# Kernel tuning notes

Measured on AMD Instinct MI355X. Metric: run time of the kernel, lower is better.

## Reference

```python
import jax, jax.numpy as jnp
import numpy as np

NUM_HEADS = 16
HEAD_SIZE = 64
ROPE_THETA = 10000.0


def _rope_tables(T, dim):
    # freqs_cis equivalent: cos/sin tables of shape [T, dim//2]
    inv_freq = 1.0 / (ROPE_THETA ** (jnp.arange(0, dim, 2, dtype=jnp.float32) / dim))
    angle = jnp.arange(T, dtype=jnp.float32)[:, None] * inv_freq[None, :]  # [T, dim/2]
    return jnp.cos(angle), jnp.sin(angle)


def _apply_rope(x, cos, sin):
    # x: [B, H, T, D]; interleaved pairs rotated by angle (complex multiply)
    x2 = x.reshape(*x.shape[:-1], -1, 2)  # [B,H,T,D/2,2]
    x0, x1 = x2[..., 0], x2[..., 1]
    c = cos[None, None, :, :]
    s = sin[None, None, :, :]
    r0 = x0 * c - x1 * s
    r1 = x0 * s + x1 * c
    return jnp.stack([r0, r1], axis=-1).reshape(x.shape)


def setup_inputs() -> dict:
    key = jax.random.key(0)
    ks = jax.random.split(key, 6)
    B, T, C = 4, 2048, 1024
    scale = 1.0 / np.sqrt(C)
    return {
        "x": jax.random.normal(ks[0], (B, T, C), dtype=jnp.float32),
        "Wq": jax.random.normal(ks[1], (C, C), dtype=jnp.float32) * scale,
        "Wk": jax.random.normal(ks[2], (C, C), dtype=jnp.float32) * scale,
        "Wv": jax.random.normal(ks[3], (C, C), dtype=jnp.float32) * scale,
        "Wo": jax.random.normal(ks[4], (C, C), dtype=jnp.float32) * scale,
        "bo": jax.random.normal(ks[5], (C,), dtype=jnp.float32) * 0.01,
    }


def reference(x, Wq, Wk, Wv, Wo, bo):
    B, T, C = x.shape
    H, D = NUM_HEADS, HEAD_SIZE
    # QKV projections (bias-free), split heads -> [B, H, T, D]
    q = (x @ Wq).reshape(B, T, H, D).transpose(0, 2, 1, 3)
    k = (x @ Wk).reshape(B, T, H, D).transpose(0, 2, 1, 3)
    v = (x @ Wv).reshape(B, T, H, D).transpose(0, 2, 1, 3)
    cos, sin = _rope_tables(T, D)
    q = _apply_rope(q, cos, sin)
    k = _apply_rope(k, cos, sin)
    # causal attention with manual stable softmax
    scores = jnp.einsum("bhqd,bhkd->bhqk", q, k) * (D ** -0.5)
    causal = jnp.tril(jnp.ones((T, T), dtype=bool))
    scores = jnp.where(causal[None, None], scores, -jnp.inf)
    probs = jax.nn.softmax(scores, axis=-1)
    out = jnp.einsum("bhqk,bhkd->bhqd", probs, v)  # [B,H,T,D]
    out = out.transpose(0, 2, 1, 3).reshape(B, T, C)
    return out @ Wo + bo
```

## Files before the change

kernel.cpp:

```cpp
#include <hip/hip_runtime.h>
#include <math.h>

#define HH 16
#define DD 64
#define TT 2048
#define BB 4
#define CC 1024
#define MM (BB*TT)

typedef __attribute__((ext_vector_type(8))) short short8;
typedef __attribute__((ext_vector_type(4))) float f32x4;
typedef __attribute__((ext_vector_type(8))) unsigned short bfu8;
typedef __attribute__((ext_vector_type(4))) unsigned short bfu4;

__device__ __forceinline__ unsigned short f2bf(float f) {
    unsigned int u = __builtin_bit_cast(unsigned int, f);
    unsigned int r = (u + 0x7fffu + ((u >> 16) & 1u)) >> 16;
    return (unsigned short)r;
}
__device__ __forceinline__ float bf2f(unsigned short s) {
    unsigned int u = ((unsigned int)s) << 16;
    return __builtin_bit_cast(float, u);
}

__global__ __launch_bounds__(256) void convert_x(
    const float* __restrict__ x, unsigned short* __restrict__ xb)
{
    const size_t i = (size_t)blockIdx.x * 256 + threadIdx.x;
    const float4 a = ((const float4*)x)[i * 2];
    const float4 b = ((const float4*)x)[i * 2 + 1];
    bfu8 o;
    o[0] = f2bf(a.x); o[1] = f2bf(a.y); o[2] = f2bf(a.z); o[3] = f2bf(a.w);
    o[4] = f2bf(b.x); o[5] = f2bf(b.y); o[6] = f2bf(b.z); o[7] = f2bf(b.w);
    *(bfu8*)(xb + i * 8) = o;
}

__global__ __launch_bounds__(256) void transpose_w(
    const float* __restrict__ Wq, const float* __restrict__ Wk,
    const float* __restrict__ Wv, const float* __restrict__ Wo,
    unsigned short* __restrict__ Wt)
{
    __shared__ float st[64][65];
    const int z = blockIdx.z;
    const float* W = (z == 0) ? Wq : (z == 1) ? Wk : (z == 2) ? Wv : Wo;
    unsigned short* out = Wt + (size_t)z * CC * CC;
    const int rb = blockIdx.y * 64, cb = blockIdx.x * 64;
    const int t = threadIdx.x;
    const int tr = t >> 4, tc4 = (t & 15) * 4;
    #pragma unroll
    for (int i = 0; i < 4; ++i) {
        const int r = i * 16 + tr;
        const float4 v = *(const float4*)&W[(size_t)(rb + r) * CC + cb + tc4];
        st[r][tc4 + 0] = v.x; st[r][tc4 + 1] = v.y;
        st[r][tc4 + 2] = v.z; st[r][tc4 + 3] = v.w;
    }
    __syncthreads();
    #pragma unroll
    for (int i = 0; i < 4; ++i) {
        const int c = i * 16 + tr;
        bfu4 o;
        o[0] = f2bf(st[tc4 + 0][c]); o[1] = f2bf(st[tc4 + 1][c]);
        o[2] = f2bf(st[tc4 + 2][c]); o[3] = f2bf(st[tc4 + 3][c]);
        *(bfu4*)&out[(size_t)(cb + c) * CC + rb + tc4] = o;
    }
}

__global__ __launch_bounds__(256) void rope_tables(float2* __restrict__ tab)
{
    const int i = blockIdx.x * 256 + threadIdx.x;
    const int t = i >> 5, p = i & 31;
    const float inv_freq = expf(-(float)(2 * p) * (9.210340371976184f / 64.0f));
    const float ang = (float)t * inv_freq;
    float s, c;
    sincosf(ang, &s, &c);
    tab[i] = make_float2(c, s);
}

__global__ __launch_bounds__(256) void transpose_v(
    const unsigned short* __restrict__ v, unsigned short* __restrict__ vt)
{
    const int bh = blockIdx.y;
    const int t  = blockIdx.x * 256 + threadIdx.x;
    const unsigned short* src = v + ((size_t)bh * TT + t) * DD;
    #pragma unroll
    for (int d0 = 0; d0 < 64; d0 += 8) {
        const bfu8 x = *(const bfu8*)(src + d0);
        #pragma unroll
        for (int j = 0; j < 8; ++j)
            vt[((size_t)bh * DD + d0 + j) * TT + t] = x[j];
    }
}

template<int MODE>
__global__ __launch_bounds__(256) void gemm_mfma(
    const unsigned short* __restrict__ A,
    const unsigned short* __restrict__ Wt,
    const float* __restrict__ bias,
    const float2* __restrict__ tab,
    void* __restrict__ outv)
{
    __shared__ short lds[128 * 32 * 2];
    short* As = lds;
    short* Bs = lds + 128 * 32;

    const int tid  = threadIdx.x;
    const int lane = tid & 63;
    const int w    = tid >> 6;
    const int wr   = w >> 1, wc = w & 1;
    const int mb   = blockIdx.y * 128, nb = blockIdx.x * 128;
    const int z    = (MODE == 1) ? blockIdx.z : 0;
    const unsigned short* Bmat = Wt + (size_t)z * CC * CC;

    f32x4 acc[4][4] = {};

    for (int k0 = 0; k0 < CC; k0 += 32) {
        __syncthreads();
        #pragma unroll
        for (int t2 = 0; t2 < 2; ++t2) {
            const int ci  = w * 128 + t2 * 64 + lane;
            const int row = ci >> 2, kc = ci & 3;
            const unsigned short* ga = A    + (size_t)(mb + row) * CC + k0 + kc * 8;
            const unsigned short* gb = Bmat + (size_t)(nb + row) * CC + k0 + kc * 8;
            __builtin_amdgcn_global_load_lds(
                (const __attribute__((address_space(1))) unsigned int*)ga,
                (__attribute__((address_space(3))) unsigned int*)(As + (w * 2 + t2) * 512),
                16, 0, 0);
            __builtin_amdgcn_global_load_lds(
                (const __attribute__((address_space(1))) unsigned int*)gb,
                (__attribute__((address_space(3))) unsigned int*)(Bs + (w * 2 + t2) * 512),
                16, 0, 0);
        }
        __syncthreads();

        short8 a[4], b[4];
        #pragma unroll
        for (int i = 0; i < 4; ++i) {
            const int ro = (wr * 64 + i * 16 + (lane & 15)) * 32 + (lane >> 4) * 8;
            a[i] = *(const short8*)&As[ro];
            const int co = (wc * 64 + i * 16 + (lane & 15)) * 32 + (lane >> 4) * 8;
            b[i] = *(const short8*)&Bs[co];
        }
        #pragma unroll
        for (int i = 0; i < 4; ++i)
            #pragma unroll
            for (int j = 0; j < 4; ++j)
                acc[i][j] = __builtin_amdgcn_mfma_f32_16x16x32_bf16(
                    a[i], b[j], acc[i][j], 0, 0, 0);
    }

    if (MODE == 0) {
        float* out = (float*)outv;
        #pragma unroll
        for (int i = 0; i < 4; ++i) {
            const int m0 = mb + wr * 64 + i * 16 + (lane >> 4) * 4;
            #pragma unroll
            for (int j = 0; j < 4; ++j) {
                const int n = nb + wc * 64 + j * 16 + (lane & 15);
                const float bv = bias[n];
                #pragma unroll
                for (int r = 0; r < 4; ++r)
                    out[(size_t)(m0 + r) * CC + n] = acc[i][j][r] + bv;
            }
        }
    } else {
        unsigned short* dst = (unsigned short*)outv + (size_t)z * MM * CC;
        const bool do_rope = (z < 2);
        #pragma unroll
        for (int i = 0; i < 4; ++i) {
            const int m0 = mb + wr * 64 + i * 16 + (lane >> 4) * 4;
            #pragma unroll
            for (int j = 0; j < 4; ++j) {
                const int n = nb + wc * 64 + j * 16 + (lane & 15);
                const int h = n >> 6, d = n & 63;
                #pragma unroll
                for (int r = 0; r < 4; ++r) {
                    const int m  = m0 + r;
                    const int b_ = m >> 11, t = m & (TT - 1);
                    const float val     = acc[i][j][r];
                    const float partner = __shfl_xor(val, 1);
                    float r0, r1;
                    if (do_rope) {
                        const float2 cs = tab[t * 32 + (d >> 1)];
                        r0 = val * cs.x - partner * cs.y;
                        r1 = val * cs.y + partner * cs.x;
                    } else {
                        r0 = val; r1 = partner;
                    }
                    if ((lane & 1) == 0) {
                        const unsigned int pk =
                            (unsigned int)f2bf(r0) | ((unsigned int)f2bf(r1) << 16);
                        *(unsigned int*)&dst[(((size_t)(b_ * HH + h) * TT + t) * DD) + (d & ~1)] = pk;
                    }
                }
            }
        }
    }
}

__global__ __launch_bounds__(256) void attn_mfma(
    const unsigned short* __restrict__ qg, const unsigned short* __restrict__ kg,
    const unsigned short* __restrict__ vtg, unsigned short* __restrict__ att)
{
    __shared__ short Ks[2][64 * 64];
    __shared__ short Vs[2][64 * 64];
    __shared__ short Ps[4][16 * 64];

    const int tid  = threadIdx.x;
    const int lane = tid & 63;
    const int w    = tid >> 6;
    const int l15  = lane & 15, l4 = lane >> 4;
    const int qt   = 31 - blockIdx.x;
    const int bh   = blockIdx.y;
    const int qb   = qt * 64;
    const int b_   = bh >> 4, h = bh & 15;

    const unsigned short* qrow = qg + ((size_t)bh * TT + qb + w * 16 + l15) * DD;
    const short8 qf0 = *(const short8*)(qrow + l4 * 8);
    const short8 qf1 = *(const short8*)(qrow + 32 + l4 * 8);

    f32x4 acc_o[4] = {};
    float m_run[4] = {-1e30f, -1e30f, -1e30f, -1e30f};
    float l_run[4] = {};

    const int srow = tid >> 2;
    const int sc0  = (tid & 3) * 16;
    const int bo0  = (srow * 128 + sc0 * 2)       ^ ((srow & 7) << 4);
    const int bo1  = (srow * 128 + (sc0 + 8) * 2) ^ ((srow & 7) << 4);
    const unsigned short* kst = kg  + ((size_t)bh * TT + srow) * DD + sc0;
    const unsigned short* vst = vtg + ((size_t)bh * DD + srow) * TT + sc0;

    const int ntile = qt + 1;

    {
        const short8 k0 = *(const short8*)(kst);
        const short8 k1 = *(const short8*)(kst + 8);
        const short8 v0 = *(const short8*)(vst);
        const short8 v1 = *(const short8*)(vst + 8);
        *(short8*)((char*)&Ks[0][0] + bo0) = k0;
        *(short8*)((char*)&Ks[0][0] + bo1) = k1;
        *(short8*)((char*)&Vs[0][0] + bo0) = v0;
        *(short8*)((char*)&Vs[0][0] + bo1) = v1;
    }
    __syncthreads();

    for (int kt = 0; kt < ntile; ++kt) {
        const int kb  = kt * 64;
        const int cur = kt & 1;
        const short* Kc = &Ks[cur][0];
        const short* Vc = &Vs[cur][0];

        short8 nk0, nk1, nv0, nv1;
        const bool has_next = (kt + 1 < ntile);
        if (has_next) {
            const size_t ko = (size_t)(kb + 64) * DD;
            nk0 = *(const short8*)(kst + ko);
            nk1 = *(const short8*)(kst + ko + 8);
            nv0 = *(const short8*)(vst + kb + 64);
            nv1 = *(const short8*)(vst + kb + 64 + 8);
        }

        f32x4 s4[4];
        __builtin_amdgcn_s_setprio(1);
        #pragma unroll
        for (int kj = 0; kj < 4; ++kj) {
            const int key = kj * 16 + l15;
            const short8 kf0 = *(const short8*)((char*)Kc + ((key * 128 +      l4 * 16) ^ ((key & 7) << 4)));
            const short8 kf1 = *(const short8*)((char*)Kc + ((key * 128 + 64 + l4 * 16) ^ ((key & 7) << 4)));
            f32x4 zz = {};
            zz = __builtin_amdgcn_mfma_f32_16x16x32_bf16(qf0, kf0, zz, 0, 0, 0);
            zz = __builtin_amdgcn_mfma_f32_16x16x32_bf16(qf1, kf1, zz, 0, 0, 0);
            s4[kj] = zz;
        }
        __builtin_amdgcn_s_setprio(0);

        float p[4][4];
        float tmax[4] = {-1e30f, -1e30f, -1e30f, -1e30f};
        const bool diag = (kt == ntile - 1);
        #pragma unroll
        for (int kj = 0; kj < 4; ++kj)
            #pragma unroll
            for (int r = 0; r < 4; ++r) {
                float s = s4[kj][r] * 0.125f;
                if (diag) {
                    const int key_g = kb + kj * 16 + l15;
                    const int q_g   = qb + w * 16 + l4 * 4 + r;
                    if (key_g > q_g) s = -1e30f;
                }
                p[kj][r] = s;
                tmax[r] = fmaxf(tmax[r], s);
            }
        #pragma unroll
        for (int mk = 1; mk < 16; mk <<= 1)
            #pragma unroll
            for (int r = 0; r < 4; ++r)
                tmax[r] = fmaxf(tmax[r], __shfl_xor(tmax[r], mk));

        #pragma unroll
        for (int r = 0; r < 4; ++r) {
            const float mn   = fmaxf(m_run[r], tmax[r]);
            const float corr = __expf(m_run[r] - mn);
            m_run[r] = mn;
            l_run[r] *= corr;
            #pragma unroll
            for (int dj = 0; dj < 4; ++dj) acc_o[dj][r] *= corr;
            float ls = 0.f;
            #pragma unroll
            for (int kj = 0; kj < 4; ++kj) {
                const float e = __expf(p[kj][r] - mn);
                p[kj][r] = e;
                ls += e;
            }
            l_run[r] += ls;
        }

        #pragma unroll
        for (int kj = 0; kj < 4; ++kj)
            #pragma unroll
            for (int r = 0; r < 4; ++r) {
                const int qr  = l4 * 4 + r;
                const int key = kj * 16 + l15;
                const int bo  = (qr * 128 + key * 2) ^ ((qr & 7) << 4);
                *(short*)((char*)&Ps[w][0] + bo) = (short)f2bf(p[kj][r]);
            }

        const short8 pa0 = *(const short8*)((char*)&Ps[w][0] + ((l15 * 128 +      l4 * 16) ^ ((l15 & 7) << 4)));
        const short8 pa1 = *(const short8*)((char*)&Ps[w][0] + ((l15 * 128 + 64 + l4 * 16) ^ ((l15 & 7) << 4)));
        __builtin_amdgcn_s_setprio(1);
        #pragma unroll
        for (int dj = 0; dj < 4; ++dj) {
            const int dr = dj * 16 + l15;
            const short8 vf0 = *(const short8*)((char*)Vc + ((dr * 128 +      l4 * 16) ^ ((dr & 7) << 4)));
            const short8 vf1 = *(const short8*)((char*)Vc + ((dr * 128 + 64 + l4 * 16) ^ ((dr & 7) << 4)));
            acc_o[dj] = __builtin_amdgcn_mfma_f32_16x16x32_bf16(pa0, vf0, acc_o[dj], 0, 0, 0);
            acc_o[dj] = __builtin_amdgcn_mfma_f32_16x16x32_bf16(pa1, vf1, acc_o[dj], 0, 0, 0);
        }
        __builtin_amdgcn_s_setprio(0);

        if (has_next) {
            char* Kn = (char*)&Ks[cur ^ 1][0];
            char* Vn = (char*)&Vs[cur ^ 1][0];
            *(short8*)(Kn + bo0) = nk0;
            *(short8*)(Kn + bo1) = nk1;
            *(short8*)(Vn + bo0) = nv0;
            *(short8*)(Vn + bo1) = nv1;
        }
        __syncthreads();
    }

    #pragma unroll
    for (int mk = 1; mk < 16; mk <<= 1)
        #pragma unroll
        for (int r = 0; r < 4; ++r)
            l_run[r] += __shfl_xor(l_run[r], mk);

    #pragma unroll
    for (int r = 0; r < 4; ++r) {
        const float inv = 1.0f / l_run[r];
        const int t = qb + w * 16 + l4 * 4 + r;
        unsigned short* orow = att + ((size_t)(b_ * TT + t)) * CC + h * DD;
        #pragma unroll
        for (int dj = 0; dj < 4; ++dj)
            orow[dj * 16 + l15] = f2bf(acc_o[dj][r] * inv);
    }
}

extern "C" void kernel_launch(void* const* d_in, const int* in_sizes, int n_in,
                              void* d_out, int out_size, void* d_ws, size_t ws_size,
                              hipStream_t stream) {
    const float* x  = (const float*)d_in[0];
    const float* Wq = (const float*)d_in[1];
    const float* Wk = (const float*)d_in[2];
    const float* Wv = (const float*)d_in[3];
    const float* Wo = (const float*)d_in[4];
    const float* bo = (const float*)d_in[5];
    float* out = (float*)d_out;

    char* ws = (char*)d_ws;
    unsigned short* xb  = (unsigned short*)ws;
    unsigned short* aw  = xb;
    unsigned short* wt  = (unsigned short*)(ws + (16ull << 20));
    unsigned short* qkv = (unsigned short*)(ws + (24ull << 20));
    unsigned short* vt  = (unsigned short*)(ws + (72ull << 20));
    float2*         tab = (float2*)       (ws + (88ull << 20));

    convert_x  <<<4096, 256, 0, stream>>>(x, xb);
    transpose_w<<<dim3(16, 16, 4), 256, 0, stream>>>(Wq, Wk, Wv, Wo, wt);
    rope_tables<<<256, 256, 0, stream>>>(tab);

    gemm_mfma<1><<<dim3(8, 64, 3), 256, 0, stream>>>(xb, wt, nullptr, tab, qkv);

    const size_t NEL = (size_t)MM * CC;
    transpose_v<<<dim3(8, 64), 256, 0, stream>>>(qkv + 2 * NEL, vt);

    attn_mfma<<<dim3(32, 64), 256, 0, stream>>>(qkv, qkv + NEL, vt, aw);

    gemm_mfma<0><<<dim3(8, 64), 256, 0, stream>>>(
        aw, wt + 3ull * CC * CC, bo, tab, out);
}
```

Baseline: 426.2 us.

## Widen attention blocks to 128 queries, lazy softmax rescale, fold scale into Q

The attention kernel now runs 512-thread blocks covering 128 query rows. Each staged K/V tile is shared by eight waves, halving global K/V traffic per query. The upper four waves skip the final tile beyond their diagonal. The online-softmax rescale of the accumulator is skipped unless some row's max grows by more than 8 (a lazy-rescale threshold). The 1/sqrt(D) scale is folded into the Q projection epilogue, removing a multiply per score. Risks are idle waves on the diagonal tiles, fewer blocks for load balance, and exponentials computed against a stale max, which relies on the threshold for numeric safety.

```diff
diff --git a/kernel.cpp b/kernel.cpp
--- a/kernel.cpp
+++ b/kernel.cpp
@@ -165,6 +165,7 @@
     } else {
         unsigned short* dst = (unsigned short*)outv + (size_t)z * MM * CC;
         const bool do_rope = (z < 2);
+        const float qscale = (z == 0) ? 0.125f : 1.0f;
         #pragma unroll
         for (int i = 0; i < 4; ++i) {
             const int m0 = mb + wr * 64 + i * 16 + (lane >> 4) * 4;
@@ -181,8 +182,8 @@
                     float r0, r1;
                     if (do_rope) {
                         const float2 cs = tab[t * 32 + (d >> 1)];
-                        r0 = val * cs.x - partner * cs.y;
-                        r1 = val * cs.y + partner * cs.x;
+                        r0 = (val * cs.x - partner * cs.y) * qscale;
+                        r1 = (val * cs.y + partner * cs.x) * qscale;
                     } else {
                         r0 = val; r1 = partner;
                     }
@@ -197,22 +198,24 @@
     }
 }
 
-__global__ __launch_bounds__(256) void attn_mfma(
+__global__ __launch_bounds__(512) void attn_mfma(
     const unsigned short* __restrict__ qg, const unsigned short* __restrict__ kg,
     const unsigned short* __restrict__ vtg, unsigned short* __restrict__ att)
 {
     __shared__ short Ks[2][64 * 64];
     __shared__ short Vs[2][64 * 64];
-    __shared__ short Ps[4][16 * 64];
+    __shared__ short Ps[8][16 * 64];
 
     const int tid  = threadIdx.x;
     const int lane = tid & 63;
     const int w    = tid >> 6;
     const int l15  = lane & 15, l4 = lane >> 4;
-    const int qt   = 31 - blockIdx.x;
+    const int jq   = 15 - blockIdx.x;
     const int bh   = blockIdx.y;
-    const int qb   = qt * 64;
+    const int qb   = jq * 128;
     const int b_   = bh >> 4, h = bh & 15;
+    const int my_diag = 2 * jq + (w >> 2);
+    const int ntile   = 2 * jq + 2;
 
     const unsigned short* qrow = qg + ((size_t)bh * TT + qb + w * 16 + l15) * DD;
     const short8 qf0 = *(const short8*)(qrow + l4 * 8);
@@ -222,24 +225,17 @@
     float m_run[4] = {-1e30f, -1e30f, -1e30f, -1e30f};
     float l_run[4] = {};
 
-    const int srow = tid >> 2;
-    const int sc0  = (tid & 3) * 16;
-    const int bo0  = (srow * 128 + sc0 * 2)       ^ ((srow & 7) << 4);
-    const int bo1  = (srow * 128 + (sc0 + 8) * 2) ^ ((srow & 7) << 4);
+    const int srow = tid >> 3;
+    const int sc0  = (tid & 7) * 8;
+    const int bo0  = (srow * 128 + sc0 * 2) ^ ((srow & 7) << 4);
     const unsigned short* kst = kg  + ((size_t)bh * TT + srow) * DD + sc0;
     const unsigned short* vst = vtg + ((size_t)bh * DD + srow) * TT + sc0;
 
-    const int ntile = qt + 1;
-
     {
         const short8 k0 = *(const short8*)(kst);
-        const short8 k1 = *(const short8*)(kst + 8);
         const short8 v0 = *(const short8*)(vst);
-        const short8 v1 = *(const short8*)(vst + 8);
         *(short8*)((char*)&Ks[0][0] + bo0) = k0;
-        *(short8*)((char*)&Ks[0][0] + bo1) = k1;
         *(short8*)((char*)&Vs[0][0] + bo0) = v0;
-        *(short8*)((char*)&Vs[0][0] + bo1) = v1;
     }
     __syncthreads();
 
@@ -249,100 +245,103 @@
         const short* Kc = &Ks[cur][0];
         const short* Vc = &Vs[cur][0];
 
-        short8 nk0, nk1, nv0, nv1;
+        short8 nk, nv;
         const bool has_next = (kt + 1 < ntile);
         if (has_next) {
-            const size_t ko = (size_t)(kb + 64) * DD;
-            nk0 = *(const short8*)(kst + ko);
-            nk1 = *(const short8*)(kst + ko + 8);
-            nv0 = *(const short8*)(vst + kb + 64);
-            nv1 = *(const short8*)(vst + kb + 64 + 8);
-        }
-
-        f32x4 s4[4];
-        __builtin_amdgcn_s_setprio(1);
-        #pragma unroll
-        for (int kj = 0; kj < 4; ++kj) {
-            const int key = kj * 16 + l15;
-            const short8 kf0 = *(const short8*)((char*)Kc + ((key * 128 +      l4 * 16) ^ ((key & 7) << 4)));
-            const short8 kf1 = *(const short8*)((char*)Kc + ((key * 128 + 64 + l4 * 16) ^ ((key & 7) << 4)));
-            f32x4 zz = {};
-            zz = __builtin_amdgcn_mfma_f32_16x16x32_bf16(qf0, kf0, zz, 0, 0, 0);
-            zz = __builtin_amdgcn_mfma_f32_16x16x32_bf16(qf1, kf1, zz, 0, 0, 0);
-            s4[kj] = zz;
-        }
-        __builtin_amdgcn_s_setprio(0);
-
-        float p[4][4];
-        float tmax[4] = {-1e30f, -1e30f, -1e30f, -1e30f};
-        const bool diag = (kt == ntile - 1);
-        #pragma unroll
-        for (int kj = 0; kj < 4; ++kj)
+            nk = *(const short8*)(kst + (size_t)(kb + 64) * DD);
+            nv = *(const short8*)(vst + kb + 64);
+        }
+
+        if (kt <= my_diag) {
+            f32x4 s4[4];
+            __builtin_amdgcn_s_setprio(1);
+            #pragma unroll
+            for (int kj = 0; kj < 4; ++kj) {
+                const int key = kj * 16 + l15;
+                const short8 kf0 = *(const short8*)((char*)Kc + ((key * 128 +      l4 * 16) ^ ((key & 7) << 4)));
+                const short8 kf1 = *(const short8*)((char*)Kc + ((key * 128 + 64 + l4 * 16) ^ ((key & 7) << 4)));
+                f32x4 zz = {};
+                zz = __builtin_amdgcn_mfma_f32_16x16x32_bf16(qf0, kf0, zz, 0, 0, 0);
+                zz = __builtin_amdgcn_mfma_f32_16x16x32_bf16(qf1, kf1, zz, 0, 0, 0);
+                s4[kj] = zz;
+            }
+            __builtin_amdgcn_s_setprio(0);
+
+            float p[4][4];
+            float tmax[4] = {-1e30f, -1e30f, -1e30f, -1e30f};
+            const bool diag = (kt == my_diag);
+            #pragma unroll
+            for (int kj = 0; kj < 4; ++kj)
+                #pragma unroll
+                for (int r = 0; r < 4; ++r) {
+                    float s = s4[kj][r];
+                    if (diag) {
+                        const int key_g = kb + kj * 16 + l15;
+                        const int q_g   = qb + w * 16 + l4 * 4 + r;
+                        if (key_g > q_g) s = -1e30f;
+                    }
+                    p[kj][r] = s;
+                    tmax[r] = fmaxf(tmax[r], s);
+                }
+            #pragma unroll
+            for (int mk = 1; mk < 16; mk <<= 1)
+                #pragma unroll
+                for (int r = 0; r < 4; ++r)
+                    tmax[r] = fmaxf(tmax[r], __shfl_xor(tmax[r], mk));
+
+            float grow = 0.f;
+            #pragma unroll
+            for (int r = 0; r < 4; ++r) grow = fmaxf(grow, tmax[r] - m_run[r]);
+            if (__any(grow > 8.f)) {
+                #pragma unroll
+                for (int r = 0; r < 4; ++r) {
+                    const float mn   = fmaxf(m_run[r], tmax[r]);
+                    const float corr = __expf(m_run[r] - mn);
+                    m_run[r] = mn;
+                    l_run[r] *= corr;
+                    #pragma unroll
+                    for (int dj = 0; dj < 4; ++dj) acc_o[dj][r] *= corr;
+                }
+            }
             #pragma unroll
             for (int r = 0; r < 4; ++r) {
-                float s = s4[kj][r] * 0.125f;
-                if (diag) {
-                    const int key_g = kb + kj * 16 + l15;
-                    const int q_g   = qb + w * 16 + l4 * 4 + r;
-                    if (key_g > q_g) s = -1e30f;
-                }
-                p[kj][r] = s;
-                tmax[r] = fmaxf(tmax[r], s);
-            }
-        #pragma unroll
-        for (int mk = 1; mk < 16; mk <<= 1)
-            #pragma unroll
-            for (int r = 0; r < 4; ++r)
-                tmax[r] = fmaxf(tmax[r], __shfl_xor(tmax[r], mk));
-
-        #pragma unroll
-        for (int r = 0; r < 4; ++r) {
-            const float mn   = fmaxf(m_run[r], tmax[r]);
-            const float corr = __expf(m_run[r] - mn);
-            m_run[r] = mn;
-            l_run[r] *= corr;
-            #pragma unroll
-            for (int dj = 0; dj < 4; ++dj) acc_o[dj][r] *= corr;
-            float ls = 0.f;
-            #pragma unroll
-            for (int kj = 0; kj < 4; ++kj) {
-                const float e = __expf(p[kj][r] - mn);
-                p[kj][r] = e;
-                ls += e;
-            }
-            l_run[r] += ls;
-        }
-
-        #pragma unroll
-        for (int kj = 0; kj < 4; ++kj)
-            #pragma unroll
-            for (int r = 0; r < 4; ++r) {
-                const int qr  = l4 * 4 + r;
-                const int key = kj * 16 + l15;
-                const int bo  = (qr * 128 + key * 2) ^ ((qr & 7) << 4);
-                *(short*)((char*)&Ps[w][0] + bo) = (short)f2bf(p[kj][r]);
-            }
-
-        const short8 pa0 = *(const short8*)((char*)&Ps[w][0] + ((l15 * 128 +      l4 * 16) ^ ((l15 & 7) << 4)));
-        const short8 pa1 = *(const short8*)((char*)&Ps[w][0] + ((l15 * 128 + 64 + l4 * 16) ^ ((l15 & 7) << 4)));
-        __builtin_amdgcn_s_setprio(1);
-        #pragma unroll
-        for (int dj = 0; dj < 4; ++dj) {
-            const int dr = dj * 16 + l15;
-            const short8 vf0 = *(const short8*)((char*)Vc + ((dr * 128 +      l4 * 16) ^ ((dr & 7) << 4)));
-            const short8 vf1 = *(const short8*)((char*)Vc + ((dr * 128 + 64 + l4 * 16) ^ ((dr & 7) << 4)));
-            acc_o[dj] = __builtin_amdgcn_mfma_f32_16x16x32_bf16(pa0, vf0, acc_o[dj], 0, 0, 0);
-            acc_o[dj] = __builtin_amdgcn_mfma_f32_16x16x32_bf16(pa1, vf1, acc_o[dj], 0, 0, 0);
-        }
-        __builtin_amdgcn_s_setprio(0);
+                float ls = 0.f;
+                #pragma unroll
+                for (int kj = 0; kj < 4; ++kj) {
+                    const float e = __expf(p[kj][r] - m_run[r]);
+                    p[kj][r] = e;
+                    ls += e;
+                }
+                l_run[r] += ls;
+            }
+
+            #pragma unroll
+            for (int kj = 0; kj < 4; ++kj)
+                #pragma unroll
+                for (int r = 0; r < 4; ++r) {
+                    const int qr  = l4 * 4 + r;
+                    const int key = kj * 16 + l15;
+                    const int bo  = (qr * 128 + key * 2) ^ ((qr & 7) << 4);
+                    *(short*)((char*)&Ps[w][0] + bo) = (short)f2bf(p[kj][r]);
+                }
+
+            const short8 pa0 = *(const short8*)((char*)&Ps[w][0] + ((l15 * 128 +      l4 * 16) ^ ((l15 & 7) << 4)));
+            const short8 pa1 = *(const short8*)((char*)&Ps[w][0] + ((l15 * 128 + 64 + l4 * 16) ^ ((l15 & 7) << 4)));
+            __builtin_amdgcn_s_setprio(1);
+            #pragma unroll
+            for (int dj = 0; dj < 4; ++dj) {
+                const int dr = dj * 16 + l15;
+                const short8 vf0 = *(const short8*)((char*)Vc + ((dr * 128 +      l4 * 16) ^ ((dr & 7) << 4)));
+                const short8 vf1 = *(const short8*)((char*)Vc + ((dr * 128 + 64 + l4 * 16) ^ ((dr & 7) << 4)));
+                acc_o[dj] = __builtin_amdgcn_mfma_f32_16x16x32_bf16(pa0, vf0, acc_o[dj], 0, 0, 0);
+                acc_o[dj] = __builtin_amdgcn_mfma_f32_16x16x32_bf16(pa1, vf1, acc_o[dj], 0, 0, 0);
+            }
+            __builtin_amdgcn_s_setprio(0);
+        }
 
         if (has_next) {
-            char* Kn = (char*)&Ks[cur ^ 1][0];
-            char* Vn = (char*)&Vs[cur ^ 1][0];
-            *(short8*)(Kn + bo0) = nk0;
-            *(short8*)(Kn + bo1) = nk1;
-            *(short8*)(Vn + bo0) = nv0;
-            *(short8*)(Vn + bo1) = nv1;
+            *(short8*)((char*)&Ks[cur ^ 1][0] + bo0) = nk;
+            *(short8*)((char*)&Vs[cur ^ 1][0] + bo0) = nv;
         }
         __syncthreads();
     }
@@ -392,7 +391,7 @@
     const size_t NEL = (size_t)MM * CC;
     transpose_v<<<dim3(8, 64), 256, 0, stream>>>(qkv + 2 * NEL, vt);
 
-    attn_mfma<<<dim3(32, 64), 256, 0, stream>>>(qkv, qkv + NEL, vt, aw);
+    attn_mfma<<<dim3(16, 64), 512, 0, stream>>>(qkv, qkv + NEL, vt, aw);
 
     gemm_mfma<0><<<dim3(8, 64), 256, 0, stream>>>(
         aw, wt + 3ull * CC * CC, bo, tab, out);
```

After: 409.4 us. 1.04x faster.
